# Performance work log

Measured on AMD Instinct MI355X. Metric: run time of the kernel, lower is better.

## Reference

```python
import jax, jax.numpy as jnp
import numpy as np

B, H, N, D = 1, 8, 2048, 64  # n >> d: fastmax's intended long-seq / small-head-dim regime


def setup_inputs() -> dict:
    key = jax.random.key(0)
    kq, kk, kv, kr = jax.random.split(key, 4)
    q = jax.random.normal(kq, (B, H, N, D), dtype=jnp.float32)
    k = jax.random.normal(kk, (B, H, N, D), dtype=jnp.float32)
    v = jax.random.normal(kv, (B, H, N, D), dtype=jnp.float32)
    rpe_matrix = jax.random.normal(kr, (2 * N - 1, D), dtype=jnp.float32)
    return {"q": q, "k": k, "v": v, "rpe_matrix": rpe_matrix, "mask": 1}


def reference(q, k, v, rpe_matrix, mask):
    # Fastmax: 2nd-order Taylor approximation of softmax attention,
    # weight(i,j) = 1 + s_ij + s_ij^2 / 2 where s_ij = q_i . (k_j) + q_i . rpe[i-j+n-1],
    # normalized by the row-sum, optionally causal (mask).
    b, h, n, d = q.shape
    # content scores: (b,h,n,n)
    s = jnp.einsum('bhid,bhjd->bhij', q, k)
    # RPE scores: project q onto every relative-position embedding, then gather
    # the (i,j) -> i-j+n-1 diagonal structure.  qr: (b,h,n,2n-1)
    qr = jnp.einsum('bhid,md->bhim', q, rpe_matrix)
    i = jnp.arange(n)[:, None]
    j = jnp.arange(n)[None, :]
    rel = i - j + (n - 1)  # (n,n) in [0, 2n-2]
    s = s + jnp.take_along_axis(qr, rel[None, None], axis=-1)
    # Taylor-2 exp approximation
    w = 1.0 + s + 0.5 * s * s
    if mask:  # causal
        w = jnp.where(j <= i, w, 0.0)
    denom = jnp.sum(w, axis=-1, keepdims=True)  # (b,h,n,1)
    out = jnp.einsum('bhij,bhjd->bhid', w, v) / denom
    return out
```

## Files before the change

### kernel.cpp

```cpp
#include <hip/hip_runtime.h>
#include <hip/hip_bf16.h>

#define HH 8
#define NN 2048
#define DD 64

typedef __attribute__((ext_vector_type(8))) short bf16x8;
typedef __attribute__((ext_vector_type(4))) float f32x4;
typedef __attribute__((ext_vector_type(8))) unsigned short u16x8;
typedef unsigned short ushort_t;

static __device__ __forceinline__ unsigned short f2bf(float x) {
    union { float f; unsigned u; } un; un.f = x;
    unsigned r = un.u + 0x7FFFu + ((un.u >> 16) & 1u);
    return (unsigned short)(r >> 16);
}
static __device__ __forceinline__ unsigned short f2bf_t(float x) {
    union { float f; unsigned u; } un; un.f = x;
    return (unsigned short)(un.u >> 16);
}
static __device__ __forceinline__ float bf2f(unsigned short u) {
    union { unsigned u; float f; } un; un.u = ((unsigned)u) << 16;
    return un.f;
}

#define OFF_Q  0u
#define OFF_K  2097152u
#define OFF_VT 4194304u
#define OFF_R  6291456u
#define OFF_P  6815744u
#define WS_NEED 24641536u

__global__ void pre_kernel(const float* __restrict__ q, const float* __restrict__ k,
                           const float* __restrict__ r, const float* __restrict__ v,
                           ushort_t* __restrict__ ws) {
    __shared__ __align__(16) ushort_t T[64][72];
    const int tid = threadIdx.x;
    const int b = blockIdx.x;
    if (b < 2304) {
        const float* srcrow;
        char* dst;
        if (b < 1024) {
            int head = b >> 7, tile = b & 127;
            srcrow = q + ((size_t)head * NN + (size_t)tile * 16) * DD;
            dst = (char*)ws + OFF_Q + (size_t)head * 262144 + (size_t)tile * 2048;
        } else if (b < 2048) {
            int bb = b - 1024; int head = bb >> 7, tile = bb & 127;
            srcrow = k + ((size_t)head * NN + (size_t)tile * 16) * DD;
            dst = (char*)ws + OFF_K + (size_t)head * 262144 + (size_t)tile * 2048;
        } else {
            int tile = b - 2048;
            srcrow = (const float*)0;
            dst = (char*)ws + OFF_R + (size_t)tile * 2048;
            int rr = tid >> 4, dc = (tid & 15) << 2;
            int row = tile * 16 + rr; if (row > 4094) row = 4094;
            float4 f = *(const float4*)&r[(size_t)row * DD + dc];
            T[rr][dc + 0] = f2bf(f.x); T[rr][dc + 1] = f2bf(f.y);
            T[rr][dc + 2] = f2bf(f.z); T[rr][dc + 3] = f2bf(f.w);
            __syncthreads();
            if (tid < 128) {
                int dh = tid >> 6, l = tid & 63, lq = l >> 4, ln = l & 15;
                u16x8 x = *(const u16x8*)&T[ln][32 * dh + 8 * lq];
                *(u16x8*)(dst + dh * 1024 + l * 16) = x;
            }
            return;
        }
        {
            int rr = tid >> 4, dc = (tid & 15) << 2;
            float4 f = *(const float4*)&srcrow[(size_t)rr * DD + dc];
            T[rr][dc + 0] = f2bf(f.x); T[rr][dc + 1] = f2bf(f.y);
            T[rr][dc + 2] = f2bf(f.z); T[rr][dc + 3] = f2bf(f.w);
        }
        __syncthreads();
        if (tid < 128) {
            int dh = tid >> 6, l = tid & 63, lq = l >> 4, ln = l & 15;
            u16x8 x = *(const u16x8*)&T[ln][32 * dh + 8 * lq];
            *(u16x8*)(dst + dh * 1024 + l * 16) = x;
        }
    } else {
        const int c = b - 2304;
        const int h = c >> 5;
        const int n0 = (c & 31) * 64;
        const float* vh = v + (size_t)h * NN * DD;
        #pragma unroll
        for (int p = 0; p < 4; ++p) {
            int c2 = tid + 256 * p; int rr = c2 >> 4, dc = (c2 & 15) << 2;
            float4 f = *(const float4*)&vh[(size_t)(n0 + rr) * DD + dc];
            T[dc + 0][rr] = f2bf(f.x); T[dc + 1][rr] = f2bf(f.y);
            T[dc + 2][rr] = f2bf(f.z); T[dc + 3][rr] = f2bf(f.w);
        }
        __syncthreads();
        char* vtb = (char*)ws + OFF_VT + (size_t)h * 262144 + (size_t)(c & 31) * 8192;
        #pragma unroll
        for (int k2 = 0; k2 < 2; ++k2) {
            int si = tid + 256 * k2;
            int jh = si >> 8, s = (si >> 6) & 3, l2 = si & 63;
            int lq2 = l2 >> 4, ln2 = l2 & 15;
            u16x8 x = *(const u16x8*)&T[16 * s + ln2][32 * jh + 8 * lq2];
            *(u16x8*)(vtb + (jh * 4 + s) * 1024 + l2 * 16) = x;
        }
    }
}

__global__ __launch_bounds__(256, 4)
void fastmax_main(const ushort_t* __restrict__ wsb, float* __restrict__ outg,
                  float* __restrict__ wsPart)
{
    __shared__ __align__(16) unsigned char U[12800];
    float* Epi = (float*)U;
    (void)outg;

    const char* qT = (const char*)wsb + OFF_Q;
    const char* kT = (const char*)wsb + OFF_K;
    const char* vT = (const char*)wsb + OFF_VT;
    const char* rT = (const char*)wsb + OFF_R;

    const int tid = threadIdx.x;
    const int w   = tid >> 6;
    const int l   = tid & 63;
    const int lq  = l >> 4;
    const int ln  = l & 15;
    const int rt  = w & 1;
    const int ch  = w >> 1;
    const int lane16 = l * 16;

    ushort_t* tsW = (ushort_t*)(U + w * 1920);
    ushort_t* wsW = (ushort_t*)(U + 7680 + w * 1280);

    const int head = blockIdx.x & 7;
    const int rest = blockIdx.x >> 3;
    const int p    = rest & 31;
    const int sub  = rest >> 5;
    const int tileA = 63 - p;
    const int njtA  = (tileA >> 1) + 1;
    const int tileB = p;

    const int lo = (33 * sub + 3) >> 2;
    const int hi = (sub == 3) ? 33 : ((33 * (sub + 1) + 3) >> 2);

    const char* qh = qT + (size_t)head * 262144;
    const char* kh = kT + (size_t)head * 262144;
    const char* vh = vT + (size_t)head * 262144;

    const int sw = 16 * rt - 32 * ch + 32;
    const int stream = head * 32 + p;

    #pragma unroll 1
    for (int seg = 0; seg < 2; ++seg) {
        int tile, jlo, jhi;
        if (seg == 0) { tile = tileA; jlo = lo; jhi = (hi < njtA) ? hi : njtA; }
        else          { tile = tileB; jlo = (lo > njtA ? lo : njtA) - njtA; jhi = hi - njtA; }
        if (jlo >= jhi) continue;
        const int i0 = tile * 32;

        const char* qp = qh + (size_t)((i0 >> 4) + rt) * 2048 + lane16;
        bf16x8 qf0 = *(const bf16x8*)(qp);
        bf16x8 qf1 = *(const bf16x8*)(qp + 1024);

        const char* kp = kh + (size_t)(jlo * 4 + 2 * ch) * 2048 + lane16;
        const char* vp = vh + (size_t)(jlo * 2 + ch) * 4096 + lane16;
        const char* rp = rT + (size_t)(((i0 - jlo * 64 + 1984 + sw) >> 4)) * 2048 + lane16;

        f32x4 acc0 = {0,0,0,0}, acc1 = {0,0,0,0}, acc2 = {0,0,0,0}, acc3 = {0,0,0,0};
        float denv0 = 0.f, denv1 = 0.f, denv2 = 0.f, denv3 = 0.f;

        #pragma unroll 1
        for (int jt = jlo; jt < jhi; ++jt) {
            const int j0 = jt * 64;

            bf16x8 b00 = *(const bf16x8*)(kp);
            bf16x8 b01 = *(const bf16x8*)(kp + 1024);
            bf16x8 b10 = *(const bf16x8*)(kp + 2048);
            bf16x8 b11 = *(const bf16x8*)(kp + 3072);
            bf16x8 e0a = *(const bf16x8*)(rp);
            bf16x8 e0b = *(const bf16x8*)(rp + 1024);
            bf16x8 e1a = *(const bf16x8*)(rp + 2048);
            bf16x8 e1b = *(const bf16x8*)(rp + 3072);
            bf16x8 e2a = *(const bf16x8*)(rp + 4096);
            bf16x8 e2b = *(const bf16x8*)(rp + 5120);
            bf16x8 v0  = *(const bf16x8*)(vp);
            bf16x8 v1  = *(const bf16x8*)(vp + 1024);
            bf16x8 v2  = *(const bf16x8*)(vp + 2048);
            bf16x8 v3  = *(const bf16x8*)(vp + 3072);
            kp += 8192; vp += 8192; rp -= 8192;

            f32x4 s0 = {0,0,0,0}, s1 = {0,0,0,0};
            s0 = __builtin_amdgcn_mfma_f32_16x16x32_bf16(qf0, b00, s0, 0, 0, 0);
            s0 = __builtin_amdgcn_mfma_f32_16x16x32_bf16(qf1, b01, s0, 0, 0, 0);
            s1 = __builtin_amdgcn_mfma_f32_16x16x32_bf16(qf0, b10, s1, 0, 0, 0);
            s1 = __builtin_amdgcn_mfma_f32_16x16x32_bf16(qf1, b11, s1, 0, 0, 0);

            {
                f32x4 t = {0,0,0,0};
                t = __builtin_amdgcn_mfma_f32_16x16x32_bf16(qf0, e0a, t, 0, 0, 0);
                t = __builtin_amdgcn_mfma_f32_16x16x32_bf16(qf1, e0b, t, 0, 0, 0);
                ushort4 pk;
                pk.x = f2bf_t(t[0]); pk.y = f2bf_t(t[1]); pk.z = f2bf_t(t[2]); pk.w = f2bf_t(t[3]);
                *(ushort4*)&tsW[(ln) * 20 + 4 * lq] = pk;
            }
            {
                f32x4 t = {0,0,0,0};
                t = __builtin_amdgcn_mfma_f32_16x16x32_bf16(qf0, e1a, t, 0, 0, 0);
                t = __builtin_amdgcn_mfma_f32_16x16x32_bf16(qf1, e1b, t, 0, 0, 0);
                ushort4 pk;
                pk.x = f2bf_t(t[0]); pk.y = f2bf_t(t[1]); pk.z = f2bf_t(t[2]); pk.w = f2bf_t(t[3]);
                *(ushort4*)&tsW[(16 + ln) * 20 + 4 * lq] = pk;
            }
            {
                f32x4 t = {0,0,0,0};
                t = __builtin_amdgcn_mfma_f32_16x16x32_bf16(qf0, e2a, t, 0, 0, 0);
                t = __builtin_amdgcn_mfma_f32_16x16x32_bf16(qf1, e2b, t, 0, 0, 0);
                ushort4 pk;
                pk.x = f2bf_t(t[0]); pk.y = f2bf_t(t[1]); pk.z = f2bf_t(t[2]); pk.w = f2bf_t(t[3]);
                *(ushort4*)&tsW[(32 + ln) * 20 + 4 * lq] = pk;
            }

            #pragma unroll
            for (int ct = 0; ct < 2; ++ct) {
                f32x4 sv = ct ? s1 : s0;
                #pragma unroll
                for (int e = 0; e < 4; ++e) {
                    int rp2 = 4 * lq + e;
                    int cp = 16 * ct + ln;
                    int bw = rp2 - cp + 31;
                    float s = sv[e] + bf2f(tsW[bw * 20 + rp2]);
                    float wv = 1.0f + s + 0.5f * s * s;
                    if (j0 + 32 * ch + cp > i0 + 16 * rt + rp2) wv = 0.0f;
                    union { float f; unsigned u; } uw; uw.f = wv;
                    wsW[rp2 * 40 + cp] = (ushort_t)(uw.u >> 16);
                    uw.u &= 0xffff0000u;
                    if (e == 0) denv0 += uw.f; else if (e == 1) denv1 += uw.f;
                    else if (e == 2) denv2 += uw.f; else denv3 += uw.f;
                }
            }

            {
                bf16x8 af = *(const bf16x8*)&wsW[ln * 40 + 8 * lq];
                acc0 = __builtin_amdgcn_mfma_f32_16x16x32_bf16(af, v0, acc0, 0, 0, 0);
                acc1 = __builtin_amdgcn_mfma_f32_16x16x32_bf16(af, v1, acc1, 0, 0, 0);
                acc2 = __builtin_amdgcn_mfma_f32_16x16x32_bf16(af, v2, acc2, 0, 0, 0);
                acc3 = __builtin_amdgcn_mfma_f32_16x16x32_bf16(af, v3, acc3, 0, 0, 0);
            }
        }

        #pragma unroll
        for (int off = 1; off <= 8; off <<= 1) {
            denv0 += __shfl_xor(denv0, off);
            denv1 += __shfl_xor(denv1, off);
            denv2 += __shfl_xor(denv2, off);
            denv3 += __shfl_xor(denv3, off);
        }

        __syncthreads();
        if (ch == 0) {
            #pragma unroll
            for (int e = 0; e < 4; ++e) {
                int r = 16 * rt + 4 * lq + e;
                Epi[r * 68 +  0 + ln] = acc0[e];
                Epi[r * 68 + 16 + ln] = acc1[e];
                Epi[r * 68 + 32 + ln] = acc2[e];
                Epi[r * 68 + 48 + ln] = acc3[e];
            }
            if (ln == 0) {
                Epi[(16 * rt + 4 * lq + 0) * 68 + 64] = denv0;
                Epi[(16 * rt + 4 * lq + 1) * 68 + 64] = denv1;
                Epi[(16 * rt + 4 * lq + 2) * 68 + 64] = denv2;
                Epi[(16 * rt + 4 * lq + 3) * 68 + 64] = denv3;
            }
        }
        __syncthreads();
        if (ch == 1) {
            #pragma unroll
            for (int e = 0; e < 4; ++e) {
                int r = 16 * rt + 4 * lq + e;
                Epi[r * 68 +  0 + ln] += acc0[e];
                Epi[r * 68 + 16 + ln] += acc1[e];
                Epi[r * 68 + 32 + ln] += acc2[e];
                Epi[r * 68 + 48 + ln] += acc3[e];
            }
            if (ln == 0) {
                Epi[(16 * rt + 4 * lq + 0) * 68 + 64] += denv0;
                Epi[(16 * rt + 4 * lq + 1) * 68 + 64] += denv1;
                Epi[(16 * rt + 4 * lq + 2) * 68 + 64] += denv2;
                Epi[(16 * rt + 4 * lq + 3) * 68 + 64] += denv3;
            }
        }
        __syncthreads();
        {
            float* dst = wsPart + ((size_t)((stream * 2 + seg) * 4 + sub)) * (32 * 68);
            for (int idx = tid; idx < 32 * 68; idx += 256) dst[idx] = Epi[idx];
        }
        __syncthreads();
    }
}

__global__ void combine_kernel(const float* __restrict__ wsPart, float* __restrict__ outg) {
    const int blk = blockIdx.x;
    const int head = blk >> 5;
    const int p = blk & 31;
    const int njtA = ((63 - p) >> 1) + 1;
    float* oh = outg + (size_t)head * NN * DD;
    #pragma unroll 1
    for (int tsel = 0; tsel < 2; ++tsel) {
        const int tile = tsel ? p : (63 - p);
        const float* base = wsPart + ((size_t)(blk * 2 + tsel)) * 4 * (32 * 68);
        int vmask = 0;
        #pragma unroll
        for (int s = 0; s < 4; ++s) {
            int lo_s = (33 * s + 3) >> 2;
            int hi_s = (s == 3) ? 33 : ((33 * (s + 1) + 3) >> 2);
            bool valid = tsel ? (hi_s > njtA) : (lo_s < njtA);
            if (valid) vmask |= 1 << s;
        }
        #pragma unroll
        for (int e2 = 0; e2 < 8; ++e2) {
            int idx = threadIdx.x + 256 * e2;
            int r = idx >> 6, d = idx & 63;
            float num = 0.f, den = 0.f;
            #pragma unroll
            for (int s = 0; s < 4; ++s) {
                if (vmask & (1 << s)) {
                    num += base[s * 2176 + r * 68 + d];
                    den += base[s * 2176 + r * 68 + 64];
                }
            }
            oh[(size_t)(tile * 32 + r) * DD + d] = num / den;
        }
    }
}

__global__ __launch_bounds__(256, 2)
void fastmax_fallback(const float* __restrict__ qg0, const float* __restrict__ kg0,
                      const float* __restrict__ vg0, const float* __restrict__ rg,
                      float* __restrict__ outg)
{
    __shared__ __align__(16) ushort_t Qs[32][72];
    __shared__ __align__(16) ushort_t Ks2[64][72];
    __shared__ __align__(16) ushort_t Bs2[96][72];
    __shared__ __align__(16) ushort_t Vts2[96][72];
    __shared__ __align__(16) float    Tsf[32][97];
    __shared__ __align__(16) ushort_t Wsf[32][72];
    __shared__ float denomLds[32];

    const int tid = threadIdx.x;
    const int w = tid >> 6, l = tid & 63, lq = l >> 4, ln = l & 15;
    const int head = blockIdx.x & 7, ib = blockIdx.x >> 3;
    const int it = 63 - ib, i0 = it * 32, njt = (it >> 1) + 1;
    const float* qg = qg0 + (size_t)head * NN * DD;
    const float* kg = kg0 + (size_t)head * NN * DD;
    const float* vg = vg0 + (size_t)head * NN * DD;
    float* og = outg + (size_t)head * NN * DD;
    {
        #pragma unroll
        for (int p = 0; p < 2; ++p) {
            int c = tid + 256 * p; int r = c >> 4, dc = (c & 15) << 2;
            float4 f = *(const float4*)&qg[(size_t)(i0 + r) * DD + dc];
            ushort4 u; u.x = f2bf(f.x); u.y = f2bf(f.y); u.z = f2bf(f.z); u.w = f2bf(f.w);
            *(ushort4*)&Qs[r][dc] = u;
        }
        for (int idx = tid; idx < 32 * 72; idx += 256) {
            int rr = idx / 72, cc = idx - rr * 72;
            Vts2[64 + rr][cc] = (rr == 0) ? (ushort_t)0x3F80 : (ushort_t)0;
        }
    }
    f32x4 a0 = {0,0,0,0}, a1 = {0,0,0,0}, a2 = {0,0,0,0};
    const int pr = w & 1, rt = w & 1, cp = w >> 1;
    for (int jt = 0; jt < njt; ++jt) {
        const int j0 = jt * 64;
        __syncthreads();
        #pragma unroll
        for (int p = 0; p < 4; ++p) {
            int c = tid + 256 * p; int r = c >> 4, dc = (c & 15) << 2;
            float4 f = *(const float4*)&kg[(size_t)(j0 + r) * DD + dc];
            ushort4 u; u.x = f2bf(f.x); u.y = f2bf(f.y); u.z = f2bf(f.z); u.w = f2bf(f.w);
            *(ushort4*)&Ks2[r][dc] = u;
        }
        const int relbase = i0 - j0 + 1984;
        #pragma unroll
        for (int p = 0; p < 6; ++p) {
            int c = tid + 256 * p; int r = c >> 4, dc = (c & 15) << 2;
            int row = relbase + r; if (row > 4094) row = 4094;
            float4 f = *(const float4*)&rg[(size_t)row * DD + dc];
            ushort4 u; u.x = f2bf(f.x); u.y = f2bf(f.y); u.z = f2bf(f.z); u.w = f2bf(f.w);
            *(ushort4*)&Bs2[r][dc] = u;
        }
        #pragma unroll
        for (int p = 0; p < 4; ++p) {
            int c = tid + 256 * p; int r = c >> 4, dc = (c & 15) << 2;
            float4 f = *(const float4*)&vg[(size_t)(j0 + r) * DD + dc];
            Vts2[dc + 0][r] = f2bf(f.x); Vts2[dc + 1][r] = f2bf(f.y);
            Vts2[dc + 2][r] = f2bf(f.z); Vts2[dc + 3][r] = f2bf(f.w);
        }
        __syncthreads();
        f32x4 s0 = {0,0,0,0}, s1 = {0,0,0,0};
        #pragma unroll
        for (int ks = 0; ks < 2; ++ks) {
            bf16x8 a = *(const bf16x8*)&Qs[16 * rt + ln][32 * ks + 8 * lq];
            bf16x8 b0 = *(const bf16x8*)&Ks2[32 * cp + ln][32 * ks + 8 * lq];
            bf16x8 b1 = *(const bf16x8*)&Ks2[32 * cp + 16 + ln][32 * ks + 8 * lq];
            s0 = __builtin_amdgcn_mfma_f32_16x16x32_bf16(a, b0, s0, 0, 0, 0);
            s1 = __builtin_amdgcn_mfma_f32_16x16x32_bf16(a, b1, s1, 0, 0, 0);
        }
        #pragma unroll
        for (int kk = 0; kk < 3; ++kk) {
            int bt = (w >> 1) + 2 * kk;
            f32x4 t = {0,0,0,0};
            #pragma unroll
            for (int ks = 0; ks < 2; ++ks) {
                bf16x8 a = *(const bf16x8*)&Qs[16 * rt + ln][32 * ks + 8 * lq];
                bf16x8 b = *(const bf16x8*)&Bs2[16 * bt + ln][32 * ks + 8 * lq];
                t = __builtin_amdgcn_mfma_f32_16x16x32_bf16(a, b, t, 0, 0, 0);
            }
            #pragma unroll
            for (int e = 0; e < 4; ++e) Tsf[16 * rt + 4 * lq + e][16 * bt + ln] = t[e];
        }
        __syncthreads();
        #pragma unroll
        for (int ct2 = 0; ct2 < 2; ++ct2) {
            f32x4 sv = ct2 ? s1 : s0;
            int c_loc = 32 * cp + 16 * ct2 + ln, j = j0 + c_loc;
            #pragma unroll
            for (int e = 0; e < 4; ++e) {
                int r_loc = 16 * rt + 4 * lq + e, i = i0 + r_loc;
                float s = sv[e] + Tsf[r_loc][r_loc - c_loc + 63];
                float wv = 1.0f + s + 0.5f * s * s;
                if (j > i) wv = 0.0f;
                Wsf[r_loc][c_loc] = f2bf(wv);
            }
        }
        __syncthreads();
        {
            bf16x8 af0 = *(const bf16x8*)&Wsf[16 * pr + ln][ 0 + 8 * lq];
            bf16x8 af1 = *(const bf16x8*)&Wsf[16 * pr + ln][32 + 8 * lq];
            int pn0 = w >> 1; bf16x8 b;
            b = *(const bf16x8*)&Vts2[16 * (pn0 + 0) + ln][ 0 + 8 * lq];
            a0 = __builtin_amdgcn_mfma_f32_16x16x32_bf16(af0, b, a0, 0, 0, 0);
            b = *(const bf16x8*)&Vts2[16 * (pn0 + 0) + ln][32 + 8 * lq];
            a0 = __builtin_amdgcn_mfma_f32_16x16x32_bf16(af1, b, a0, 0, 0, 0);
            b = *(const bf16x8*)&Vts2[16 * (pn0 + 2) + ln][ 0 + 8 * lq];
            a1 = __builtin_amdgcn_mfma_f32_16x16x32_bf16(af0, b, a1, 0, 0, 0);
            b = *(const bf16x8*)&Vts2[16 * (pn0 + 2) + ln][32 + 8 * lq];
            a1 = __builtin_amdgcn_mfma_f32_16x16x32_bf16(af1, b, a1, 0, 0, 0);
            b = *(const bf16x8*)&Vts2[16 * (pn0 + 4) + ln][ 0 + 8 * lq];
            a2 = __builtin_amdgcn_mfma_f32_16x16x32_bf16(af0, b, a2, 0, 0, 0);
            b = *(const bf16x8*)&Vts2[16 * (pn0 + 4) + ln][32 + 8 * lq];
            a2 = __builtin_amdgcn_mfma_f32_16x16x32_bf16(af1, b, a2, 0, 0, 0);
        }
    }
    if (w < 2 && ln == 0) {
        #pragma unroll
        for (int e = 0; e < 4; ++e) denomLds[16 * pr + 4 * lq + e] = a2[e];
    }
    __syncthreads();
    #pragma unroll
    for (int k = 0; k < 2; ++k) {
        int pn = (w >> 1) + 2 * k;
        f32x4 acc = k ? a1 : a0;
        #pragma unroll
        for (int e = 0; e < 4; ++e) {
            int r_loc = 16 * pr + 4 * lq + e;
            og[(size_t)(i0 + r_loc) * DD + 16 * pn + ln] = acc[e] / denomLds[r_loc];
        }
    }
}

extern "C" void kernel_launch(void* const* d_in, const int* in_sizes, int n_in,
                              void* d_out, int out_size, void* d_ws, size_t ws_size,
                              hipStream_t stream) {
    const float* q   = (const float*)d_in[0];
    const float* k   = (const float*)d_in[1];
    const float* v   = (const float*)d_in[2];
    const float* rpe = (const float*)d_in[3];
    float* out = (float*)d_out;

    if (ws_size >= WS_NEED) {
        ushort_t* wsb = (ushort_t*)d_ws;
        float* wsPart = (float*)((char*)d_ws + OFF_P);
        hipLaunchKernelGGL(pre_kernel, dim3(2560), dim3(256), 0, stream,
                           q, k, rpe, v, wsb);
        hipLaunchKernelGGL(fastmax_main, dim3(1024), dim3(256), 0, stream,
                           wsb, out, wsPart);
        hipLaunchKernelGGL(combine_kernel, dim3(256), dim3(256), 0, stream, wsPart, out);
    } else {
        hipLaunchKernelGGL(fastmax_fallback, dim3(512), dim3(256), 0, stream,
                           q, k, v, rpe, out);
    }
}
```

Before: 106.3 us.

## Fuse preprocess, attention and combine into one cooperative kernel with grid syncs

Merges the three launches (bf16 conversion/transpose, main attention, partial combine) into one cooperative kernel of 1024 blocks. Two grid-wide syncs separate the phases, which removes launch gaps between kernels. The combine step is also split over 512 blocks instead of 256. The old three-kernel path stays as a fallback if the cooperative launch fails. The trade-off is grid-sync cost and a residency requirement of 1024 blocks at 4 per CU, plus a lower WS_NEED threshold.

```diff
diff --git a/kernel.cpp b/kernel.cpp
--- a/kernel.cpp
+++ b/kernel.cpp
@@ -1,5 +1,8 @@
 #include <hip/hip_runtime.h>
 #include <hip/hip_bf16.h>
+#include <hip/hip_cooperative_groups.h>
+
+namespace cg = cooperative_groups;
 
 #define HH 8
 #define NN 2048
@@ -29,7 +32,300 @@
 #define OFF_VT 4194304u
 #define OFF_R  6291456u
 #define OFF_P  6815744u
-#define WS_NEED 24641536u
+#define WS_NEED 11272192u
+
+__global__ __launch_bounds__(256, 4)
+void fastmax_fused(const float* __restrict__ qg, const float* __restrict__ kg,
+                   const float* __restrict__ rg, const float* __restrict__ vg,
+                   ushort_t* __restrict__ ws, float* __restrict__ outg)
+{
+    __shared__ __align__(16) unsigned char U[12800];
+    const int tid = threadIdx.x;
+
+    {
+        ushort_t (*T)[72] = (ushort_t (*)[72])U;
+        #pragma unroll 1
+        for (int ob = blockIdx.x; ob < 2560; ob += 1024) {
+            __syncthreads();
+            if (ob < 2304) {
+                char* dst;
+                float4 f;
+                const int rr = tid >> 4, dc = (tid & 15) << 2;
+                if (ob < 1024) {
+                    int head = ob >> 7, tile = ob & 127;
+                    const float* srcrow = qg + ((size_t)head * NN + (size_t)tile * 16) * DD;
+                    dst = (char*)ws + OFF_Q + (size_t)head * 262144 + (size_t)tile * 2048;
+                    f = *(const float4*)&srcrow[(size_t)rr * DD + dc];
+                } else if (ob < 2048) {
+                    int bb = ob - 1024; int head = bb >> 7, tile = bb & 127;
+                    const float* srcrow = kg + ((size_t)head * NN + (size_t)tile * 16) * DD;
+                    dst = (char*)ws + OFF_K + (size_t)head * 262144 + (size_t)tile * 2048;
+                    f = *(const float4*)&srcrow[(size_t)rr * DD + dc];
+                } else {
+                    int tile = ob - 2048;
+                    dst = (char*)ws + OFF_R + (size_t)tile * 2048;
+                    int row = tile * 16 + rr; if (row > 4094) row = 4094;
+                    f = *(const float4*)&rg[(size_t)row * DD + dc];
+                }
+                T[rr][dc + 0] = f2bf(f.x); T[rr][dc + 1] = f2bf(f.y);
+                T[rr][dc + 2] = f2bf(f.z); T[rr][dc + 3] = f2bf(f.w);
+                __syncthreads();
+                if (tid < 128) {
+                    int dh = tid >> 6, l2 = tid & 63, lq2 = l2 >> 4, ln2 = l2 & 15;
+                    u16x8 x = *(const u16x8*)&T[ln2][32 * dh + 8 * lq2];
+                    *(u16x8*)(dst + dh * 1024 + l2 * 16) = x;
+                }
+            } else {
+                const int c = ob - 2304;
+                const int h = c >> 5;
+                const int n0 = (c & 31) * 64;
+                const float* vh = vg + (size_t)h * NN * DD;
+                #pragma unroll
+                for (int p2 = 0; p2 < 4; ++p2) {
+                    int c2 = tid + 256 * p2; int rr2 = c2 >> 4, dc2 = (c2 & 15) << 2;
+                    float4 f2 = *(const float4*)&vh[(size_t)(n0 + rr2) * DD + dc2];
+                    T[dc2 + 0][rr2] = f2bf(f2.x); T[dc2 + 1][rr2] = f2bf(f2.y);
+                    T[dc2 + 2][rr2] = f2bf(f2.z); T[dc2 + 3][rr2] = f2bf(f2.w);
+                }
+                __syncthreads();
+                char* vtb = (char*)ws + OFF_VT + (size_t)h * 262144 + (size_t)(c & 31) * 8192;
+                #pragma unroll
+                for (int k2 = 0; k2 < 2; ++k2) {
+                    int si = tid + 256 * k2;
+                    int jh = si >> 8, s2 = (si >> 6) & 3, l2 = si & 63;
+                    int lq2 = l2 >> 4, ln2 = l2 & 15;
+                    u16x8 x = *(const u16x8*)&T[16 * s2 + ln2][32 * jh + 8 * lq2];
+                    *(u16x8*)(vtb + (jh * 4 + s2) * 1024 + l2 * 16) = x;
+                }
+            }
+        }
+    }
+
+    cg::this_grid().sync();
+
+    {
+        float* Epi = (float*)U;
+        float* wsPart = (float*)((char*)ws + OFF_P);
+
+        const char* qT = (const char*)ws + OFF_Q;
+        const char* kT = (const char*)ws + OFF_K;
+        const char* vT = (const char*)ws + OFF_VT;
+        const char* rT = (const char*)ws + OFF_R;
+
+        const int w   = tid >> 6;
+        const int l   = tid & 63;
+        const int lq  = l >> 4;
+        const int ln  = l & 15;
+        const int rt  = w & 1;
+        const int ch  = w >> 1;
+        const int lane16 = l * 16;
+
+        ushort_t* tsW = (ushort_t*)(U + w * 1920);
+        ushort_t* wsW = (ushort_t*)(U + 7680 + w * 1280);
+
+        const int head = blockIdx.x & 7;
+        const int rest = blockIdx.x >> 3;
+        const int p    = rest & 31;
+        const int sub  = rest >> 5;
+        const int tileA = 63 - p;
+        const int njtA  = (tileA >> 1) + 1;
+        const int tileB = p;
+
+        const int lo = (33 * sub + 3) >> 2;
+        const int hi = (sub == 3) ? 33 : ((33 * (sub + 1) + 3) >> 2);
+
+        const char* qh = qT + (size_t)head * 262144;
+        const char* kh = kT + (size_t)head * 262144;
+        const char* vh = vT + (size_t)head * 262144;
+
+        const int sw = 16 * rt - 32 * ch + 32;
+        const int stream = head * 32 + p;
+
+        #pragma unroll 1
+        for (int seg = 0; seg < 2; ++seg) {
+            int tile, jlo, jhi;
+            if (seg == 0) { tile = tileA; jlo = lo; jhi = (hi < njtA) ? hi : njtA; }
+            else          { tile = tileB; jlo = (lo > njtA ? lo : njtA) - njtA; jhi = hi - njtA; }
+            if (jlo >= jhi) continue;
+            const int i0 = tile * 32;
+
+            const char* qp = qh + (size_t)((i0 >> 4) + rt) * 2048 + lane16;
+            bf16x8 qf0 = *(const bf16x8*)(qp);
+            bf16x8 qf1 = *(const bf16x8*)(qp + 1024);
+
+            const char* kp = kh + (size_t)(jlo * 4 + 2 * ch) * 2048 + lane16;
+            const char* vp = vh + (size_t)(jlo * 2 + ch) * 4096 + lane16;
+            const char* rp = rT + (size_t)(((i0 - jlo * 64 + 1984 + sw) >> 4)) * 2048 + lane16;
+
+            f32x4 acc0 = {0,0,0,0}, acc1 = {0,0,0,0}, acc2 = {0,0,0,0}, acc3 = {0,0,0,0};
+            float denv0 = 0.f, denv1 = 0.f, denv2 = 0.f, denv3 = 0.f;
+
+            #pragma unroll 1
+            for (int jt = jlo; jt < jhi; ++jt) {
+                const int j0 = jt * 64;
+
+                bf16x8 b00 = *(const bf16x8*)(kp);
+                bf16x8 b01 = *(const bf16x8*)(kp + 1024);
+                bf16x8 b10 = *(const bf16x8*)(kp + 2048);
+                bf16x8 b11 = *(const bf16x8*)(kp + 3072);
+                bf16x8 e0a = *(const bf16x8*)(rp);
+                bf16x8 e0b = *(const bf16x8*)(rp + 1024);
+                bf16x8 e1a = *(const bf16x8*)(rp + 2048);
+                bf16x8 e1b = *(const bf16x8*)(rp + 3072);
+                bf16x8 e2a = *(const bf16x8*)(rp + 4096);
+                bf16x8 e2b = *(const bf16x8*)(rp + 5120);
+                bf16x8 v0  = *(const bf16x8*)(vp);
+                bf16x8 v1  = *(const bf16x8*)(vp + 1024);
+                bf16x8 v2  = *(const bf16x8*)(vp + 2048);
+                bf16x8 v3  = *(const bf16x8*)(vp + 3072);
+                kp += 8192; vp += 8192; rp -= 8192;
+
+                f32x4 s0 = {0,0,0,0}, s1 = {0,0,0,0};
+                s0 = __builtin_amdgcn_mfma_f32_16x16x32_bf16(qf0, b00, s0, 0, 0, 0);
+                s0 = __builtin_amdgcn_mfma_f32_16x16x32_bf16(qf1, b01, s0, 0, 0, 0);
+                s1 = __builtin_amdgcn_mfma_f32_16x16x32_bf16(qf0, b10, s1, 0, 0, 0);
+                s1 = __builtin_amdgcn_mfma_f32_16x16x32_bf16(qf1, b11, s1, 0, 0, 0);
+
+                {
+                    f32x4 t = {0,0,0,0};
+                    t = __builtin_amdgcn_mfma_f32_16x16x32_bf16(qf0, e0a, t, 0, 0, 0);
+                    t = __builtin_amdgcn_mfma_f32_16x16x32_bf16(qf1, e0b, t, 0, 0, 0);
+                    ushort4 pk;
+                    pk.x = f2bf_t(t[0]); pk.y = f2bf_t(t[1]); pk.z = f2bf_t(t[2]); pk.w = f2bf_t(t[3]);
+                    *(ushort4*)&tsW[(ln) * 20 + 4 * lq] = pk;
+                }
+                {
+                    f32x4 t = {0,0,0,0};
+                    t = __builtin_amdgcn_mfma_f32_16x16x32_bf16(qf0, e1a, t, 0, 0, 0);
+                    t = __builtin_amdgcn_mfma_f32_16x16x32_bf16(qf1, e1b, t, 0, 0, 0);
+                    ushort4 pk;
+                    pk.x = f2bf_t(t[0]); pk.y = f2bf_t(t[1]); pk.z = f2bf_t(t[2]); pk.w = f2bf_t(t[3]);
+                    *(ushort4*)&tsW[(16 + ln) * 20 + 4 * lq] = pk;
+                }
+                {
+                    f32x4 t = {0,0,0,0};
+                    t = __builtin_amdgcn_mfma_f32_16x16x32_bf16(qf0, e2a, t, 0, 0, 0);
+                    t = __builtin_amdgcn_mfma_f32_16x16x32_bf16(qf1, e2b, t, 0, 0, 0);
+                    ushort4 pk;
+                    pk.x = f2bf_t(t[0]); pk.y = f2bf_t(t[1]); pk.z = f2bf_t(t[2]); pk.w = f2bf_t(t[3]);
+                    *(ushort4*)&tsW[(32 + ln) * 20 + 4 * lq] = pk;
+                }
+
+                #pragma unroll
+                for (int ct = 0; ct < 2; ++ct) {
+                    f32x4 sv = ct ? s1 : s0;
+                    #pragma unroll
+                    for (int e = 0; e < 4; ++e) {
+                        int rp2 = 4 * lq + e;
+                        int cp = 16 * ct + ln;
+                        int bw = rp2 - cp + 31;
+                        float s = sv[e] + bf2f(tsW[bw * 20 + rp2]);
+                        float wv = 1.0f + s + 0.5f * s * s;
+                        if (j0 + 32 * ch + cp > i0 + 16 * rt + rp2) wv = 0.0f;
+                        union { float f; unsigned u; } uw; uw.f = wv;
+                        wsW[rp2 * 40 + cp] = (ushort_t)(uw.u >> 16);
+                        uw.u &= 0xffff0000u;
+                        if (e == 0) denv0 += uw.f; else if (e == 1) denv1 += uw.f;
+                        else if (e == 2) denv2 += uw.f; else denv3 += uw.f;
+                    }
+                }
+
+                {
+                    bf16x8 af = *(const bf16x8*)&wsW[ln * 40 + 8 * lq];
+                    acc0 = __builtin_amdgcn_mfma_f32_16x16x32_bf16(af, v0, acc0, 0, 0, 0);
+                    acc1 = __builtin_amdgcn_mfma_f32_16x16x32_bf16(af, v1, acc1, 0, 0, 0);
+                    acc2 = __builtin_amdgcn_mfma_f32_16x16x32_bf16(af, v2, acc2, 0, 0, 0);
+                    acc3 = __builtin_amdgcn_mfma_f32_16x16x32_bf16(af, v3, acc3, 0, 0, 0);
+                }
+            }
+
+            #pragma unroll
+            for (int off = 1; off <= 8; off <<= 1) {
+                denv0 += __shfl_xor(denv0, off);
+                denv1 += __shfl_xor(denv1, off);
+                denv2 += __shfl_xor(denv2, off);
+                denv3 += __shfl_xor(denv3, off);
+            }
+
+            __syncthreads();
+            if (ch == 0) {
+                #pragma unroll
+                for (int e = 0; e < 4; ++e) {
+                    int r = 16 * rt + 4 * lq + e;
+                    Epi[r * 68 +  0 + ln] = acc0[e];
+                    Epi[r * 68 + 16 + ln] = acc1[e];
+                    Epi[r * 68 + 32 + ln] = acc2[e];
+                    Epi[r * 68 + 48 + ln] = acc3[e];
+                }
+                if (ln == 0) {
+                    Epi[(16 * rt + 4 * lq + 0) * 68 + 64] = denv0;
+                    Epi[(16 * rt + 4 * lq + 1) * 68 + 64] = denv1;
+                    Epi[(16 * rt + 4 * lq + 2) * 68 + 64] = denv2;
+                    Epi[(16 * rt + 4 * lq + 3) * 68 + 64] = denv3;
+                }
+            }
+            __syncthreads();
+            if (ch == 1) {
+                #pragma unroll
+                for (int e = 0; e < 4; ++e) {
+                    int r = 16 * rt + 4 * lq + e;
+                    Epi[r * 68 +  0 + ln] += acc0[e];
+                    Epi[r * 68 + 16 + ln] += acc1[e];
+                    Epi[r * 68 + 32 + ln] += acc2[e];
+                    Epi[r * 68 + 48 + ln] += acc3[e];
+                }
+                if (ln == 0) {
+                    Epi[(16 * rt + 4 * lq + 0) * 68 + 64] += denv0;
+                    Epi[(16 * rt + 4 * lq + 1) * 68 + 64] += denv1;
+                    Epi[(16 * rt + 4 * lq + 2) * 68 + 64] += denv2;
+                    Epi[(16 * rt + 4 * lq + 3) * 68 + 64] += denv3;
+                }
+            }
+            __syncthreads();
+            {
+                float* dst = wsPart + ((size_t)((stream * 2 + seg) * 4 + sub)) * (32 * 68);
+                for (int idx = tid; idx < 32 * 68; idx += 256) dst[idx] = Epi[idx];
+            }
+            __syncthreads();
+        }
+    }
+
+    cg::this_grid().sync();
+
+    if (blockIdx.x < 512) {
+        const float* wsPart = (const float*)((const char*)ws + OFF_P);
+        const int blk  = blockIdx.x >> 1;
+        const int tsel = blockIdx.x & 1;
+        const int head = blk >> 5;
+        const int p = blk & 31;
+        const int njtA = ((63 - p) >> 1) + 1;
+        float* oh = outg + (size_t)head * NN * DD;
+        const int tile = tsel ? p : (63 - p);
+        const float* base = wsPart + ((size_t)(blk * 2 + tsel)) * 4 * (32 * 68);
+        int vmask = 0;
+        #pragma unroll
+        for (int s = 0; s < 4; ++s) {
+            int lo_s = (33 * s + 3) >> 2;
+            int hi_s = (s == 3) ? 33 : ((33 * (s + 1) + 3) >> 2);
+            bool valid = tsel ? (hi_s > njtA) : (lo_s < njtA);
+            if (valid) vmask |= 1 << s;
+        }
+        #pragma unroll
+        for (int e2 = 0; e2 < 8; ++e2) {
+            int idx = tid + 256 * e2;
+            int r = idx >> 6, d = idx & 63;
+            float num = 0.f, den = 0.f;
+            #pragma unroll
+            for (int s = 0; s < 4; ++s) {
+                if (vmask & (1 << s)) {
+                    num += base[s * 2176 + r * 68 + d];
+                    den += base[s * 2176 + r * 68 + 64];
+                }
+            }
+            oh[(size_t)(tile * 32 + r) * DD + d] = num / den;
+        }
+    }
+}
 
 __global__ void pre_kernel(const float* __restrict__ q, const float* __restrict__ k,
                            const float* __restrict__ r, const float* __restrict__ v,
@@ -38,39 +334,27 @@
     const int tid = threadIdx.x;
     const int b = blockIdx.x;
     if (b < 2304) {
-        const float* srcrow;
         char* dst;
+        float4 f;
+        const int rr = tid >> 4, dc = (tid & 15) << 2;
         if (b < 1024) {
             int head = b >> 7, tile = b & 127;
-            srcrow = q + ((size_t)head * NN + (size_t)tile * 16) * DD;
+            const float* srcrow = q + ((size_t)head * NN + (size_t)tile * 16) * DD;
             dst = (char*)ws + OFF_Q + (size_t)head * 262144 + (size_t)tile * 2048;
+            f = *(const float4*)&srcrow[(size_t)rr * DD + dc];
         } else if (b < 2048) {
             int bb = b - 1024; int head = bb >> 7, tile = bb & 127;
-            srcrow = k + ((size_t)head * NN + (size_t)tile * 16) * DD;
+            const float* srcrow = k + ((size_t)head * NN + (size_t)tile * 16) * DD;
             dst = (char*)ws + OFF_K + (size_t)head * 262144 + (size_t)tile * 2048;
+            f = *(const float4*)&srcrow[(size_t)rr * DD + dc];
         } else {
             int tile = b - 2048;
-            srcrow = (const float*)0;
             dst = (char*)ws + OFF_R + (size_t)tile * 2048;
-            int rr = tid >> 4, dc = (tid & 15) << 2;
             int row = tile * 16 + rr; if (row > 4094) row = 4094;
-            float4 f = *(const float4*)&r[(size_t)row * DD + dc];
-            T[rr][dc + 0] = f2bf(f.x); T[rr][dc + 1] = f2bf(f.y);
-            T[rr][dc + 2] = f2bf(f.z); T[rr][dc + 3] = f2bf(f.w);
-            __syncthreads();
-            if (tid < 128) {
-                int dh = tid >> 6, l = tid & 63, lq = l >> 4, ln = l & 15;
-                u16x8 x = *(const u16x8*)&T[ln][32 * dh + 8 * lq];
-                *(u16x8*)(dst + dh * 1024 + l * 16) = x;
-            }
-            return;
-        }
-        {
-            int rr = tid >> 4, dc = (tid & 15) << 2;
-            float4 f = *(const float4*)&srcrow[(size_t)rr * DD + dc];
-            T[rr][dc + 0] = f2bf(f.x); T[rr][dc + 1] = f2bf(f.y);
-            T[rr][dc + 2] = f2bf(f.z); T[rr][dc + 3] = f2bf(f.w);
-        }
+            f = *(const float4*)&r[(size_t)row * DD + dc];
+        }
+        T[rr][dc + 0] = f2bf(f.x); T[rr][dc + 1] = f2bf(f.y);
+        T[rr][dc + 2] = f2bf(f.z); T[rr][dc + 3] = f2bf(f.w);
         __syncthreads();
         if (tid < 128) {
             int dh = tid >> 6, l = tid & 63, lq = l >> 4, ln = l & 15;
@@ -167,7 +451,6 @@
         #pragma unroll 1
         for (int jt = jlo; jt < jhi; ++jt) {
             const int j0 = jt * 64;
-
             bf16x8 b00 = *(const bf16x8*)(kp);
             bf16x8 b01 = *(const bf16x8*)(kp + 1024);
             bf16x8 b10 = *(const bf16x8*)(kp + 2048);
@@ -295,37 +578,35 @@
 }
 
 __global__ void combine_kernel(const float* __restrict__ wsPart, float* __restrict__ outg) {
-    const int blk = blockIdx.x;
+    const int blk  = blockIdx.x >> 1;
+    const int tsel = blockIdx.x & 1;
     const int head = blk >> 5;
     const int p = blk & 31;
     const int njtA = ((63 - p) >> 1) + 1;
     float* oh = outg + (size_t)head * NN * DD;
-    #pragma unroll 1
-    for (int tsel = 0; tsel < 2; ++tsel) {
-        const int tile = tsel ? p : (63 - p);
-        const float* base = wsPart + ((size_t)(blk * 2 + tsel)) * 4 * (32 * 68);
-        int vmask = 0;
+    const int tile = tsel ? p : (63 - p);
+    const float* base = wsPart + ((size_t)(blk * 2 + tsel)) * 4 * (32 * 68);
+    int vmask = 0;
+    #pragma unroll
+    for (int s = 0; s < 4; ++s) {
+        int lo_s = (33 * s + 3) >> 2;
+        int hi_s = (s == 3) ? 33 : ((33 * (s + 1) + 3) >> 2);
+        bool valid = tsel ? (hi_s > njtA) : (lo_s < njtA);
+        if (valid) vmask |= 1 << s;
+    }
+    #pragma unroll
+    for (int e2 = 0; e2 < 8; ++e2) {
+        int idx = threadIdx.x + 256 * e2;
+        int r = idx >> 6, d = idx & 63;
+        float num = 0.f, den = 0.f;
         #pragma unroll
         for (int s = 0; s < 4; ++s) {
-            int lo_s = (33 * s + 3) >> 2;
-            int hi_s = (s == 3) ? 33 : ((33 * (s + 1) + 3) >> 2);
-            bool valid = tsel ? (hi_s > njtA) : (lo_s < njtA);
-            if (valid) vmask |= 1 << s;
-        }
-        #pragma unroll
-        for (int e2 = 0; e2 < 8; ++e2) {
-            int idx = threadIdx.x + 256 * e2;
-            int r = idx >> 6, d = idx & 63;
-            float num = 0.f, den = 0.f;
-            #pragma unroll
-            for (int s = 0; s < 4; ++s) {
-                if (vmask & (1 << s)) {
-                    num += base[s * 2176 + r * 68 + d];
-                    den += base[s * 2176 + r * 68 + 64];
-                }
-            }
-            oh[(size_t)(tile * 32 + r) * DD + d] = num / den;
-        }
+            if (vmask & (1 << s)) {
+                num += base[s * 2176 + r * 68 + d];
+                den += base[s * 2176 + r * 68 + 64];
+            }
+        }
+        oh[(size_t)(tile * 32 + r) * DD + d] = num / den;
     }
 }
 
@@ -476,11 +757,19 @@
     if (ws_size >= WS_NEED) {
         ushort_t* wsb = (ushort_t*)d_ws;
         float* wsPart = (float*)((char*)d_ws + OFF_P);
-        hipLaunchKernelGGL(pre_kernel, dim3(2560), dim3(256), 0, stream,
-                           q, k, rpe, v, wsb);
-        hipLaunchKernelGGL(fastmax_main, dim3(1024), dim3(256), 0, stream,
-                           wsb, out, wsPart);
-        hipLaunchKernelGGL(combine_kernel, dim3(256), dim3(256), 0, stream, wsPart, out);
+        void* kargs[] = { (void*)&q, (void*)&k, (void*)&rpe, (void*)&v,
+                          (void*)&wsb, (void*)&out };
+        hipError_t err = hipLaunchCooperativeKernel((void*)fastmax_fused,
+                                                    dim3(1024), dim3(256),
+                                                    kargs, 0, stream);
+        if (err != hipSuccess) {
+            (void)hipGetLastError();
+            hipLaunchKernelGGL(pre_kernel, dim3(2560), dim3(256), 0, stream,
+                               q, k, rpe, v, wsb);
+            hipLaunchKernelGGL(fastmax_main, dim3(1024), dim3(256), 0, stream,
+                               wsb, out, wsPart);
+            hipLaunchKernelGGL(combine_kernel, dim3(512), dim3(256), 0, stream, wsPart, out);
+        }
     } else {
         hipLaunchKernelGGL(fastmax_fallback, dim3(512), dim3(256), 0, stream,
                            q, k, v, rpe, out);
```

Result: slower. 358.0 us (+236.9%).

## Gather RPE diagonal scores via lane shuffles instead of LDS round-trip

Applied to the files above, without the earlier changes.

The RPE projection tiles are no longer written to shared memory as bf16 and read back along diagonals. Each lane now fetches the needed diagonal element from registers with cross-lane shuffles and selects between adjacent tiles based on row/column position. This removes an LDS store/load per element and shrinks shared memory per block, and it keeps the RPE term in fp32 instead of truncating it to bf16. Separately, the combine kernel is split across twice as many blocks (one per tile) and the pre-kernel branches are unified.

```diff
diff --git a/kernel.cpp b/kernel.cpp
--- a/kernel.cpp
+++ b/kernel.cpp
@@ -14,10 +14,6 @@
     union { float f; unsigned u; } un; un.f = x;
     unsigned r = un.u + 0x7FFFu + ((un.u >> 16) & 1u);
     return (unsigned short)(r >> 16);
-}
-static __device__ __forceinline__ unsigned short f2bf_t(float x) {
-    union { float f; unsigned u; } un; un.f = x;
-    return (unsigned short)(un.u >> 16);
 }
 static __device__ __forceinline__ float bf2f(unsigned short u) {
     union { unsigned u; float f; } un; un.u = ((unsigned)u) << 16;
@@ -38,39 +34,27 @@
     const int tid = threadIdx.x;
     const int b = blockIdx.x;
     if (b < 2304) {
-        const float* srcrow;
         char* dst;
+        float4 f;
+        const int rr = tid >> 4, dc = (tid & 15) << 2;
         if (b < 1024) {
             int head = b >> 7, tile = b & 127;
-            srcrow = q + ((size_t)head * NN + (size_t)tile * 16) * DD;
+            const float* srcrow = q + ((size_t)head * NN + (size_t)tile * 16) * DD;
             dst = (char*)ws + OFF_Q + (size_t)head * 262144 + (size_t)tile * 2048;
+            f = *(const float4*)&srcrow[(size_t)rr * DD + dc];
         } else if (b < 2048) {
             int bb = b - 1024; int head = bb >> 7, tile = bb & 127;
-            srcrow = k + ((size_t)head * NN + (size_t)tile * 16) * DD;
+            const float* srcrow = k + ((size_t)head * NN + (size_t)tile * 16) * DD;
             dst = (char*)ws + OFF_K + (size_t)head * 262144 + (size_t)tile * 2048;
+            f = *(const float4*)&srcrow[(size_t)rr * DD + dc];
         } else {
             int tile = b - 2048;
-            srcrow = (const float*)0;
             dst = (char*)ws + OFF_R + (size_t)tile * 2048;
-            int rr = tid >> 4, dc = (tid & 15) << 2;
             int row = tile * 16 + rr; if (row > 4094) row = 4094;
-            float4 f = *(const float4*)&r[(size_t)row * DD + dc];
-            T[rr][dc + 0] = f2bf(f.x); T[rr][dc + 1] = f2bf(f.y);
-            T[rr][dc + 2] = f2bf(f.z); T[rr][dc + 3] = f2bf(f.w);
-            __syncthreads();
-            if (tid < 128) {
-                int dh = tid >> 6, l = tid & 63, lq = l >> 4, ln = l & 15;
-                u16x8 x = *(const u16x8*)&T[ln][32 * dh + 8 * lq];
-                *(u16x8*)(dst + dh * 1024 + l * 16) = x;
-            }
-            return;
-        }
-        {
-            int rr = tid >> 4, dc = (tid & 15) << 2;
-            float4 f = *(const float4*)&srcrow[(size_t)rr * DD + dc];
-            T[rr][dc + 0] = f2bf(f.x); T[rr][dc + 1] = f2bf(f.y);
-            T[rr][dc + 2] = f2bf(f.z); T[rr][dc + 3] = f2bf(f.w);
-        }
+            f = *(const float4*)&r[(size_t)row * DD + dc];
+        }
+        T[rr][dc + 0] = f2bf(f.x); T[rr][dc + 1] = f2bf(f.y);
+        T[rr][dc + 2] = f2bf(f.z); T[rr][dc + 3] = f2bf(f.w);
         __syncthreads();
         if (tid < 128) {
             int dh = tid >> 6, l = tid & 63, lq = l >> 4, ln = l & 15;
@@ -106,7 +90,7 @@
 void fastmax_main(const ushort_t* __restrict__ wsb, float* __restrict__ outg,
                   float* __restrict__ wsPart)
 {
-    __shared__ __align__(16) unsigned char U[12800];
+    __shared__ __align__(16) unsigned char U[8704];
     float* Epi = (float*)U;
     (void)outg;
 
@@ -124,8 +108,7 @@
     const int ch  = w >> 1;
     const int lane16 = l * 16;
 
-    ushort_t* tsW = (ushort_t*)(U + w * 1920);
-    ushort_t* wsW = (ushort_t*)(U + 7680 + w * 1280);
+    ushort_t* wsW = (ushort_t*)(U + w * 1280);
 
     const int head = blockIdx.x & 7;
     const int rest = blockIdx.x >> 3;
@@ -190,48 +173,37 @@
             s1 = __builtin_amdgcn_mfma_f32_16x16x32_bf16(qf0, b10, s1, 0, 0, 0);
             s1 = __builtin_amdgcn_mfma_f32_16x16x32_bf16(qf1, b11, s1, 0, 0, 0);
 
-            {
-                f32x4 t = {0,0,0,0};
-                t = __builtin_amdgcn_mfma_f32_16x16x32_bf16(qf0, e0a, t, 0, 0, 0);
-                t = __builtin_amdgcn_mfma_f32_16x16x32_bf16(qf1, e0b, t, 0, 0, 0);
-                ushort4 pk;
-                pk.x = f2bf_t(t[0]); pk.y = f2bf_t(t[1]); pk.z = f2bf_t(t[2]); pk.w = f2bf_t(t[3]);
-                *(ushort4*)&tsW[(ln) * 20 + 4 * lq] = pk;
-            }
-            {
-                f32x4 t = {0,0,0,0};
-                t = __builtin_amdgcn_mfma_f32_16x16x32_bf16(qf0, e1a, t, 0, 0, 0);
-                t = __builtin_amdgcn_mfma_f32_16x16x32_bf16(qf1, e1b, t, 0, 0, 0);
-                ushort4 pk;
-                pk.x = f2bf_t(t[0]); pk.y = f2bf_t(t[1]); pk.z = f2bf_t(t[2]); pk.w = f2bf_t(t[3]);
-                *(ushort4*)&tsW[(16 + ln) * 20 + 4 * lq] = pk;
-            }
-            {
-                f32x4 t = {0,0,0,0};
-                t = __builtin_amdgcn_mfma_f32_16x16x32_bf16(qf0, e2a, t, 0, 0, 0);
-                t = __builtin_amdgcn_mfma_f32_16x16x32_bf16(qf1, e2b, t, 0, 0, 0);
-                ushort4 pk;
-                pk.x = f2bf_t(t[0]); pk.y = f2bf_t(t[1]); pk.z = f2bf_t(t[2]); pk.w = f2bf_t(t[3]);
-                *(ushort4*)&tsW[(32 + ln) * 20 + 4 * lq] = pk;
-            }
-
-            #pragma unroll
-            for (int ct = 0; ct < 2; ++ct) {
-                f32x4 sv = ct ? s1 : s0;
-                #pragma unroll
-                for (int e = 0; e < 4; ++e) {
-                    int rp2 = 4 * lq + e;
-                    int cp = 16 * ct + ln;
-                    int bw = rp2 - cp + 31;
-                    float s = sv[e] + bf2f(tsW[bw * 20 + rp2]);
-                    float wv = 1.0f + s + 0.5f * s * s;
-                    if (j0 + 32 * ch + cp > i0 + 16 * rt + rp2) wv = 0.0f;
-                    union { float f; unsigned u; } uw; uw.f = wv;
-                    wsW[rp2 * 40 + cp] = (ushort_t)(uw.u >> 16);
-                    uw.u &= 0xffff0000u;
-                    if (e == 0) denv0 += uw.f; else if (e == 1) denv1 += uw.f;
-                    else if (e == 2) denv2 += uw.f; else denv3 += uw.f;
-                }
+            f32x4 t0 = {0,0,0,0}, t1 = {0,0,0,0}, t2 = {0,0,0,0};
+            t0 = __builtin_amdgcn_mfma_f32_16x16x32_bf16(qf0, e0a, t0, 0, 0, 0);
+            t0 = __builtin_amdgcn_mfma_f32_16x16x32_bf16(qf1, e0b, t0, 0, 0, 0);
+            t1 = __builtin_amdgcn_mfma_f32_16x16x32_bf16(qf0, e1a, t1, 0, 0, 0);
+            t1 = __builtin_amdgcn_mfma_f32_16x16x32_bf16(qf1, e1b, t1, 0, 0, 0);
+            t2 = __builtin_amdgcn_mfma_f32_16x16x32_bf16(qf0, e2a, t2, 0, 0, 0);
+            t2 = __builtin_amdgcn_mfma_f32_16x16x32_bf16(qf1, e2b, t2, 0, 0, 0);
+
+            #pragma unroll
+            for (int e = 0; e < 4; ++e) {
+                int rp2 = 4 * lq + e;
+                int src = 16 * lq + ((rp2 - ln + 15) & 15);
+                float sh0 = __shfl(t0[e], src, 64);
+                float sh1 = __shfl(t1[e], src, 64);
+                float sh2 = __shfl(t2[e], src, 64);
+                bool cond = rp2 > ln;
+                float sA = s0[e] + (cond ? sh2 : sh1);
+                float sB = s1[e] + (cond ? sh1 : sh0);
+                float wv0 = 1.0f + sA + 0.5f * sA * sA;
+                if (j0 + 32 * ch + ln > i0 + 16 * rt + rp2) wv0 = 0.0f;
+                union { float f; unsigned u; } u0; u0.f = wv0;
+                wsW[rp2 * 40 + ln] = (ushort_t)(u0.u >> 16);
+                u0.u &= 0xffff0000u;
+                float wv1 = 1.0f + sB + 0.5f * sB * sB;
+                if (j0 + 32 * ch + 16 + ln > i0 + 16 * rt + rp2) wv1 = 0.0f;
+                union { float f; unsigned u; } u1; u1.f = wv1;
+                wsW[rp2 * 40 + 16 + ln] = (ushort_t)(u1.u >> 16);
+                u1.u &= 0xffff0000u;
+                float de = u0.f + u1.f;
+                if (e == 0) denv0 += de; else if (e == 1) denv1 += de;
+                else if (e == 2) denv2 += de; else denv3 += de;
             }
 
             {
@@ -295,37 +267,35 @@
 }
 
 __global__ void combine_kernel(const float* __restrict__ wsPart, float* __restrict__ outg) {
-    const int blk = blockIdx.x;
+    const int blk  = blockIdx.x >> 1;
+    const int tsel = blockIdx.x & 1;
     const int head = blk >> 5;
     const int p = blk & 31;
     const int njtA = ((63 - p) >> 1) + 1;
     float* oh = outg + (size_t)head * NN * DD;
-    #pragma unroll 1
-    for (int tsel = 0; tsel < 2; ++tsel) {
-        const int tile = tsel ? p : (63 - p);
-        const float* base = wsPart + ((size_t)(blk * 2 + tsel)) * 4 * (32 * 68);
-        int vmask = 0;
+    const int tile = tsel ? p : (63 - p);
+    const float* base = wsPart + ((size_t)(blk * 2 + tsel)) * 4 * (32 * 68);
+    int vmask = 0;
+    #pragma unroll
+    for (int s = 0; s < 4; ++s) {
+        int lo_s = (33 * s + 3) >> 2;
+        int hi_s = (s == 3) ? 33 : ((33 * (s + 1) + 3) >> 2);
+        bool valid = tsel ? (hi_s > njtA) : (lo_s < njtA);
+        if (valid) vmask |= 1 << s;
+    }
+    #pragma unroll
+    for (int e2 = 0; e2 < 8; ++e2) {
+        int idx = threadIdx.x + 256 * e2;
+        int r = idx >> 6, d = idx & 63;
+        float num = 0.f, den = 0.f;
         #pragma unroll
         for (int s = 0; s < 4; ++s) {
-            int lo_s = (33 * s + 3) >> 2;
-            int hi_s = (s == 3) ? 33 : ((33 * (s + 1) + 3) >> 2);
-            bool valid = tsel ? (hi_s > njtA) : (lo_s < njtA);
-            if (valid) vmask |= 1 << s;
-        }
-        #pragma unroll
-        for (int e2 = 0; e2 < 8; ++e2) {
-            int idx = threadIdx.x + 256 * e2;
-            int r = idx >> 6, d = idx & 63;
-            float num = 0.f, den = 0.f;
-            #pragma unroll
-            for (int s = 0; s < 4; ++s) {
-                if (vmask & (1 << s)) {
-                    num += base[s * 2176 + r * 68 + d];
-                    den += base[s * 2176 + r * 68 + 64];
-                }
-            }
-            oh[(size_t)(tile * 32 + r) * DD + d] = num / den;
-        }
+            if (vmask & (1 << s)) {
+                num += base[s * 2176 + r * 68 + d];
+                den += base[s * 2176 + r * 68 + 64];
+            }
+        }
+        oh[(size_t)(tile * 32 + r) * DD + d] = num / den;
     }
 }
 
@@ -480,7 +450,7 @@
                            q, k, rpe, v, wsb);
         hipLaunchKernelGGL(fastmax_main, dim3(1024), dim3(256), 0, stream,
                            wsb, out, wsPart);
-        hipLaunchKernelGGL(combine_kernel, dim3(256), dim3(256), 0, stream, wsPart, out);
+        hipLaunchKernelGGL(combine_kernel, dim3(512), dim3(256), 0, stream, wsPart, out);
     } else {
         hipLaunchKernelGGL(fastmax_fallback, dim3(512), dim3(256), 0, stream,
                            q, k, v, rpe, out);
```

Result: faster. 103.9 us (-2.3%).
